# Kernel tuning notes

Measured on AMD Instinct MI355X. Metric: run time of the kernel, lower is better.

Reference implementation:

```python
import jax, jax.numpy as jnp
import numpy as np

EPS = 1e-12
SAMPLE_SIZES = (100, 50)  # hardcoded in the torch module


def setup_inputs() -> dict:
    key = jax.random.key(0)
    k1, k2, k3, k4 = jax.random.split(key, 4)
    N, E, C_IN, C_HID, C_OUT = 50000, 1600000, 256, 64, 128
    x = jax.random.normal(k1, (N, C_IN), dtype=jnp.float32)
    edge_index = jax.random.randint(k2, (2, E), 0, N, dtype=jnp.int64)
    W1 = jax.random.normal(k3, (C_IN, C_HID), dtype=jnp.float32) / np.sqrt(C_IN)
    b1 = jnp.zeros((C_HID,), dtype=jnp.float32)
    W2 = jax.random.normal(k4, (C_HID, C_OUT), dtype=jnp.float32) / np.sqrt(C_HID)
    b2 = jnp.zeros((C_OUT,), dtype=jnp.float32)
    return {"x": x, "edge_index": edge_index, "W1": W1, "b1": b1, "W2": W2, "b2": b2}


def _sample_mask(edge_index, num_samples, key):
    """Keep at most num_samples random out-edges per source node (fixed-shape mask)."""
    src = edge_index[0]
    E = src.shape[0]
    pri = jax.random.uniform(key, (E,))
    order = jnp.lexsort((pri, src))            # group by src, random order within group
    src_sorted = src[order]
    first = jnp.searchsorted(src_sorted, src_sorted, side="left")
    rank = jnp.arange(E) - first               # rank within each src group
    keep_sorted = rank < num_samples
    mask = jnp.zeros((E,), dtype=jnp.float32).at[order].set(keep_sorted.astype(jnp.float32))
    return mask


def _gcn_conv(x, edge_index, edge_weight, W, b, num_nodes):
    """PyG GCNConv: self-loops + symmetric deg^-1/2 normalization, aggregate at dst."""
    h = x @ W                                   # [N, out]
    src, dst = edge_index[0], edge_index[1]
    loop = jnp.arange(num_nodes, dtype=src.dtype)
    src_f = jnp.concatenate([src, loop])
    dst_f = jnp.concatenate([dst, loop])
    w_f = jnp.concatenate([edge_weight, jnp.ones((num_nodes,), dtype=edge_weight.dtype)])
    deg = jax.ops.segment_sum(w_f, dst_f, num_segments=num_nodes)
    dinv = jnp.where(deg > 0, jax.lax.rsqrt(jnp.maximum(deg, EPS)), 0.0)
    norm = w_f * dinv[src_f] * dinv[dst_f]      # [E+N]
    msgs = h[src_f] * norm[:, None]             # gather + scale (memory bound)
    out = jax.ops.segment_sum(msgs, dst_f, num_segments=num_nodes)
    return out + b


def reference(x, edge_index, W1, b1, W2, b2):
    num_nodes = x.shape[0]
    skey = jax.random.key(42)
    sk1, sk2 = jax.random.split(skey)
    m1 = _sample_mask(edge_index, SAMPLE_SIZES[0], sk1)
    m2 = _sample_mask(edge_index, SAMPLE_SIZES[1], sk2)
    h = _gcn_conv(x, edge_index, m1, W1, b1, num_nodes)
    h = jax.nn.relu(h)
    h = h / jnp.maximum(jnp.linalg.norm(h, axis=-1, keepdims=True), EPS)  # F.normalize(p=2)
    out = _gcn_conv(h, edge_index, m2, W2, b2, num_nodes)
    return out
```

## Files before the change

kernel.cpp:

```cpp
#include <hip/hip_runtime.h>

typedef unsigned int u32;
typedef unsigned short u16;
typedef unsigned long long u64;
typedef __attribute__((ext_vector_type(8))) short bh8;
typedef __attribute__((ext_vector_type(4))) float f4;

#define HMAX 1024
#define MAXD 128
#define SB_CAP 24576
#define DB_CAP 6144
#define SBCHUNK 8192
#define SPLIT 8
#define G1S 72
#define DROP_CAP 32768
#define CPAD 16

__device__ inline f4 mfma16(bh8 a, bh8 b, f4 c) {
  return __builtin_amdgcn_mfma_f32_16x16x32_bf16(a, b, c, 0, 0, 0);
}

__host__ __device__ inline void tf2x32(u32 k0, u32 k1, u32 x0, u32 x1, u32& o0, u32& o1) {
  u32 ks2 = k0 ^ k1 ^ 0x1BD11BDAu;
#define ROTL32(x,d) (((x)<<(d))|((x)>>(32-(d))))
#define TFR(r) { x0 += x1; x1 = ROTL32(x1,(r)); x1 ^= x0; }
  x0 += k0; x1 += k1;
  TFR(13) TFR(15) TFR(26) TFR(6)
  x0 += k1; x1 += ks2 + 1u;
  TFR(17) TFR(29) TFR(16) TFR(24)
  x0 += ks2; x1 += k0 + 2u;
  TFR(13) TFR(15) TFR(26) TFR(6)
  x0 += k0; x1 += k1 + 3u;
  TFR(17) TFR(29) TFR(16) TFR(24)
  x0 += k1; x1 += ks2 + 4u;
  TFR(13) TFR(15) TFR(26) TFR(6)
  x0 += ks2; x1 += k0 + 5u;
  o0 = x0; o1 = x1;
#undef TFR
#undef ROTL32
}

__device__ inline u16 f2bf(float f) {
  u32 u = __float_as_uint(f);
  return (u16)((u + 0x7FFFu + ((u >> 16) & 1u)) >> 16);
}
__device__ inline float bflo(u32 u) { return __uint_as_float(u << 16); }
__device__ inline float bfhi(u32 u) { return __uint_as_float(u & 0xFFFF0000u); }

struct BinS { u32 lsrc[128]; u32 lbase[128]; u32 ldst[512]; u32 dbase[512]; };
struct GemS { u16 xs[64 * G1S]; u16 ws[64 * G1S]; };

__global__ __launch_bounds__(256) void k_mega1(const int* __restrict__ ei, int E,
                                               const float* __restrict__ x, int N,
                                               const float* __restrict__ W1, const float* __restrict__ W2,
                                               int* __restrict__ srcCnt, u32* __restrict__ srcRec,
                                               int* __restrict__ dstCnt, u64* __restrict__ dstRec,
                                               u16* __restrict__ h1b, u16* __restrict__ W2t, int nBin) {
  __shared__ __align__(16) char smem[sizeof(GemS)];
  int t = threadIdx.x;
  int bid = blockIdx.x;
  int nGemm = (N + 63) >> 6;

  if (bid < nBin) {
    BinS& S = *(BinS*)smem;
    if (t < 128) S.lsrc[t] = 0;
    for (int v = t; v < 512; v += 256) S.ldst[v] = 0;
    __syncthreads();
    int lo = bid * SBCHUNK;
    int hi = min(lo + SBCHUNK, E);
    bool fast = ((E & 3) == 0);

    auto loadE = [&](int e0, int nv, int* sv, int* dv) {
      if (nv == 8 && fast) {
        int4 a0 = *((const int4*)(ei + e0));
        int4 a1 = *((const int4*)(ei + e0 + 4));
        int4 b0 = *((const int4*)(ei + E + e0));
        int4 b1 = *((const int4*)(ei + E + e0 + 4));
        sv[0]=a0.x; sv[1]=a0.y; sv[2]=a0.z; sv[3]=a0.w; sv[4]=a1.x; sv[5]=a1.y; sv[6]=a1.z; sv[7]=a1.w;
        dv[0]=b0.x; dv[1]=b0.y; dv[2]=b0.z; dv[3]=b0.w; dv[4]=b1.x; dv[5]=b1.y; dv[6]=b1.z; dv[7]=b1.w;
      } else {
        for (int j = 0; j < nv; ++j) { sv[j] = ei[e0 + j]; dv[j] = ei[E + e0 + j]; }
      }
    };

    for (int sub = 0; sub < SBCHUNK; sub += 2048) {
      int e0 = lo + sub + 8 * t;
      int nv = min(8, hi - e0); if (nv < 0) nv = 0;
      int sv[8], dv[8];
      loadE(e0, nv, sv, dv);
      for (int j = 0; j < nv; ++j) {
        atomicAdd(&S.lsrc[sv[j] >> 9], 1u);
        atomicAdd(&S.ldst[dv[j] >> 7], 1u);
      }
    }
    __syncthreads();
    if (t < 128) {
      u32 c = S.lsrc[t];
      if (c) S.lbase[t] = (u32)atomicAdd(&srcCnt[t * CPAD], (int)c);
      S.lsrc[t] = 0;
    }
    for (int v = t; v < 512; v += 256) {
      u32 cd = S.ldst[v];
      if (cd) S.dbase[v] = (u32)atomicAdd(&dstCnt[v * CPAD], (int)cd);
      S.ldst[v] = 0;
    }
    __syncthreads();
    for (int sub = 0; sub < SBCHUNK; sub += 2048) {
      int e0 = lo + sub + 8 * t;
      int nv = min(8, hi - e0); if (nv < 0) nv = 0;
      int sv[8], dv[8];
      loadE(e0, nv, sv, dv);
      for (int j = 0; j < nv; ++j) {
        int s = sv[j], d = dv[j];
        u32 i = (u32)(e0 + j);
        int bs = s >> 9;
        u32 slot = S.lbase[bs] + atomicAdd(&S.lsrc[bs], 1u);
        if (slot < SB_CAP) srcRec[(size_t)bs * SB_CAP + slot] = ((u32)(s & 511) << 21) | i;
        int bd = d >> 7;
        u32 slot2 = S.dbase[bd] + atomicAdd(&S.ldst[bd], 1u);
        if (slot2 < DB_CAP)
          dstRec[(size_t)bd * DB_CAP + slot2] = ((u64)(d & 127) << 37) | ((u64)(u32)s << 21) | i;
      }
    }
  } else if (bid < nBin + nGemm) {
    GemS& G = *(GemS*)smem;
    int wv = t >> 6, lane = t & 63;
    int qd = lane >> 4, md = lane & 15;
    int m0 = (bid - nBin) * 64;
    if (m0 >= N) return;
    f4 acc[4] = {};
    for (int ks = 0; ks < 256; ks += 64) {
      __syncthreads();
#pragma unroll
      for (int i = 0; i < 4; ++i) {
        int f = t + 256 * i;
        int r = f >> 4, c4 = f & 15;
        int grow = m0 + r; if (grow >= N) grow = N - 1;
        float4 v = ((const float4*)x)[(size_t)grow * 64 + (ks >> 2) + c4];
        u32 p0 = (u32)f2bf(v.x) | ((u32)f2bf(v.y) << 16);
        u32 p1 = (u32)f2bf(v.z) | ((u32)f2bf(v.w) << 16);
        *((uint2*)(G.xs + r * G1S + c4 * 4)) = make_uint2(p0, p1);
      }
#pragma unroll
      for (int i = 0; i < 4; ++i) {
        int f = t + 256 * i;
        int k = f >> 4, c4 = f & 15;
        float4 v = ((const float4*)W1)[(ks + k) * 16 + c4];
        int n0 = c4 * 4;
        G.ws[(n0 + 0) * G1S + k] = f2bf(v.x);
        G.ws[(n0 + 1) * G1S + k] = f2bf(v.y);
        G.ws[(n0 + 2) * G1S + k] = f2bf(v.z);
        G.ws[(n0 + 3) * G1S + k] = f2bf(v.w);
      }
      __syncthreads();
#pragma unroll
      for (int kk = 0; kk < 64; kk += 32) {
        bh8 af = *((const bh8*)(G.xs + (16 * wv + md) * G1S + kk + qd * 8));
#pragma unroll
        for (int nt = 0; nt < 4; ++nt) {
          bh8 bf = *((const bh8*)(G.ws + (nt * 16 + md) * G1S + kk + qd * 8));
          acc[nt] = mfma16(af, bf, acc[nt]);
        }
      }
    }
#pragma unroll
    for (int nt = 0; nt < 4; ++nt)
#pragma unroll
      for (int r = 0; r < 4; ++r) {
        int row = m0 + 16 * wv + qd * 4 + r;
        if (row < N) h1b[(size_t)row * 64 + nt * 16 + md] = f2bf(acc[nt][r]);
      }
  } else {
    for (int e = t; e < 64 * 128; e += 256) {
      int n = e & 127, k = e >> 7;
      W2t[n * 64 + k] = f2bf(W2[k * 128 + n]);
    }
  }
}

__global__ __launch_bounds__(256) void k_shist(const int* __restrict__ srcCnt, const u32* __restrict__ srcRec,
                                               int* __restrict__ outdegB) {
  int bk = blockIdx.x >> 3;
  int part = blockIdx.x & (SPLIT - 1);
  int total = min(srcCnt[bk * CPAD], SB_CAP);
  int lo = total * part / SPLIT;
  int hi = total * (part + 1) / SPLIT;
  __shared__ u32 cnt[512];
  int t = threadIdx.x;
  cnt[t] = 0; cnt[t + 256] = 0;
  __syncthreads();
  const u32* R = srcRec + (size_t)bk * SB_CAP;
  for (int i = lo + t; i < hi; i += 256) atomicAdd(&cnt[R[i] >> 21], 1u);
  __syncthreads();
  int base = bk * 512;
  for (int v = t; v < 512; v += 256) {
    u32 c = cnt[v];
    if (c) atomicAdd(&outdegB[base + v], (int)c);
  }
}

__global__ __launch_bounds__(256) void k_hdetect(const int* __restrict__ outdegB, u32* __restrict__ idAB,
                                                 int* __restrict__ hcA, int* __restrict__ hcB,
                                                 const int* __restrict__ dstCnt, int* __restrict__ bucketBase,
                                                 int* __restrict__ dptr, int nbD, int N) {
  int t = threadIdx.x;
  if (blockIdx.x == 0) {
    __shared__ int sc[512], tp[512];
    for (int i = t; i < 512; i += 256) sc[i] = (i < nbD) ? min(dstCnt[i * CPAD], DB_CAP) : 0;
    __syncthreads();
    for (int off = 1; off < 512; off <<= 1) {
      for (int i = t; i < 512; i += 256) tp[i] = sc[i] + ((i >= off) ? sc[i - off] : 0);
      __syncthreads();
      for (int i = t; i < 512; i += 256) sc[i] = tp[i];
      __syncthreads();
    }
    for (int i = t; i < 512; i += 256) {
      if (i < nbD) bucketBase[i] = (i == 0) ? 0 : sc[i - 1];
    }
    if (t == 0) {
      int tot = sc[nbD - 1];
      bucketBase[nbD] = tot;
      dptr[N] = tot;
    }
  }
  int v = blockIdx.x * 256 + t;
  if (v >= N) return;
  int dg = outdegB[v];
  u32 pk = 0;
  if (dg > 50) {
    int idb = atomicAdd(hcB, 1);
    if (idb < HMAX) pk = (u32)(idb + 1);
    if (dg > 100) {
      int ida = atomicAdd(hcA, 1);
      if (ida < HMAX) pk |= (u32)(ida + 1) << 16;
    }
  }
  idAB[v] = pk;
}

__global__ __launch_bounds__(256) void k_hfill(const int* __restrict__ srcCnt, const u32* __restrict__ srcRec,
                                               const u32* __restrict__ idAB,
                                               int* __restrict__ bcA, u64* __restrict__ bukA,
                                               int* __restrict__ bcB, u64* __restrict__ bukB,
                                               u32 kaA, u32 kbA, u32 kaB, u32 kbB) {
  int bk = blockIdx.x >> 3;
  int part = blockIdx.x & (SPLIT - 1);
  int total = min(srcCnt[bk * CPAD], SB_CAP);
  int lo = total * part / SPLIT;
  int hi = total * (part + 1) / SPLIT;
  const u32* R = srcRec + (size_t)bk * SB_CAP;
  int base = bk * 512;
  for (int i = lo + threadIdx.x; i < hi; i += 256) {
    u32 r = R[i];
    u32 pk = idAB[base + (int)(r >> 21)];
    if (pk) {
      u32 e = r & 0x1FFFFFu;
      int idb = (int)(pk & 0xFFFFu) - 1;
      if (idb >= 0) {
        u32 w0, w1; tf2x32(kaB, kbB, 0u, e, w0, w1);
        int slot = atomicAdd(&bcB[idb], 1);
        if (slot < MAXD) bukB[(size_t)idb * MAXD + slot] = ((u64)((w0 ^ w1) >> 9) << 32) | e;
      }
      int ida = (int)(pk >> 16) - 1;
      if (ida >= 0) {
        u32 w0, w1; tf2x32(kaA, kbA, 0u, e, w0, w1);
        int slot = atomicAdd(&bcA[ida], 1);
        if (slot < MAXD) bukA[(size_t)ida * MAXD + slot] = ((u64)((w0 ^ w1) >> 9) << 32) | e;
      }
    }
  }
}

__global__ __launch_bounds__(256) void k_rank2(const int* __restrict__ hcA, const int* __restrict__ bcA,
                                               const u64* __restrict__ bukA,
                                               const int* __restrict__ hcB, const int* __restrict__ bcB,
                                               const u64* __restrict__ bukB,
                                               int* __restrict__ dropCnt, u32* __restrict__ dropList) {
  bool isA = blockIdx.x < (HMAX / 4);
  int bx = isA ? blockIdx.x : blockIdx.x - HMAX / 4;
  const int* hcount = isA ? hcA : hcB;
  const int* bcount = isA ? bcA : bcB;
  const u64* bucket = isA ? bukA : bukB;
  int S = isA ? 100 : 50;
  u32 bit = isA ? 1u : 2u;
  int wid = (bx * 256 + (int)threadIdx.x) >> 6;
  int lane = threadIdx.x & 63;
  int hc = hcount[0]; if (hc > HMAX) hc = HMAX;
  if (wid >= hc) return;
  int d = bcount[wid]; if (d > MAXD) d = MAXD;
  const u64* B = bucket + (size_t)wid * MAXD;
  for (int i = lane; i < d; i += 64) {
    u64 ki = B[i];
    int rank = 0;
    for (int j = 0; j < d; ++j) rank += (B[j] < ki) ? 1 : 0;
    if (rank >= S) {
      int idx = atomicAdd(dropCnt, 1);
      if (idx < DROP_CAP) dropList[idx] = ((u32)ki & 0x1FFFFFu) | (bit << 21);
    }
  }
}

__global__ __launch_bounds__(256) void k_phase2(const int* __restrict__ bucketBase,
                                                const int* __restrict__ dstCnt,
                                                const u64* __restrict__ dstRec,
                                                const int* __restrict__ dropCnt,
                                                const u32* __restrict__ dropList,
                                                u32* __restrict__ entries, int* __restrict__ dptr,
                                                float* __restrict__ dinv1, float* __restrict__ dinv2, int N) {
  int b = blockIdx.x;
  int base = bucketBase[b];
  int cnt0 = min(dstCnt[b * CPAD], DB_CAP);
  const u64* R = dstRec + (size_t)b * DB_CAP;
  __shared__ u32 cnt[128];
  __shared__ u32 htab[4096];
  __shared__ u32 ws2[2];
  int t = threadIdx.x;
  if (t < 128) cnt[t] = 0;
  for (int i = t; i < 4096; i += 256) htab[i] = 0xFFFFFFFFu;
  __syncthreads();
  int dc = min(dropCnt[0], 3072);
  for (int i = t; i < dc; i += 256) {
    u32 pk = dropList[i];
    u32 key = pk & 0x1FFFFFu;
    u32 h = (key * 2654435761u) >> 20;
    while (true) {
      u32 old = atomicCAS(&htab[h], 0xFFFFFFFFu, pk);
      if (old == 0xFFFFFFFFu) break;
      if ((old & 0x1FFFFFu) == key) { atomicOr(&htab[h], pk & 0x00600000u); break; }
      h = (h + 1) & 4095;
    }
  }
  __syncthreads();
  for (int i = t; i < cnt0; i += 256) {
    u64 r = R[i];
    u32 dl = (u32)(r >> 37) & 127u;
    u32 key = (u32)r & 0x1FFFFFu;
    u32 drop = 0;
    u32 h = (key * 2654435761u) >> 20;
    while (true) {
      u32 v = htab[h];
      if (v == 0xFFFFFFFFu) break;
      if ((v & 0x1FFFFFu) == key) { drop = (v >> 21) & 3u; break; }
      h = (h + 1) & 4095;
    }
    u32 add = 1u + ((1u - (drop & 1u)) << 10) + ((1u - ((drop >> 1) & 1u)) << 20);
    atomicAdd(&cnt[dl], add);
  }
  __syncthreads();
  u32 c0 = (t < 128) ? cnt[t] : 0;
  u32 tot = c0 & 1023u;
  int lane = t & 63, w = t >> 6;
  u32 incl = tot;
  for (int off = 1; off < 64; off <<= 1) {
    u32 nbv = (u32)__shfl_up((int)incl, off, 64);
    if (lane >= off) incl += nbv;
  }
  if (lane == 63 && w == 0) ws2[0] = incl;
  __syncthreads();
  u32 excl = incl - tot + ((w == 1) ? ws2[0] : 0u);
  int v0 = b * 128 + t;
  if (t < 128 && v0 < N) {
    dptr[v0] = base + (int)excl;
    dinv1[v0] = 1.0f / sqrtf((float)(((c0 >> 10) & 1023u) + 1u));
    dinv2[v0] = 1.0f / sqrtf((float)(((c0 >> 20) & 1023u) + 1u));
  }
  __syncthreads();
  if (t < 128) cnt[t] = excl;
  __syncthreads();
  for (int i = t; i < cnt0; i += 256) {
    u64 r = R[i];
    u32 dl = (u32)(r >> 37) & 127u;
    u32 key = (u32)r & 0x1FFFFFu;
    u32 drop = 0;
    u32 h = (key * 2654435761u) >> 20;
    while (true) {
      u32 v = htab[h];
      if (v == 0xFFFFFFFFu) break;
      if ((v & 0x1FFFFFu) == key) { drop = (v >> 21) & 3u; break; }
      h = (h + 1) & 4095;
    }
    u32 src = (u32)(r >> 21) & 0xFFFFu;
    u32 slot = atomicAdd(&cnt[dl], 1u);
    entries[base + slot] = src | ((drop & 1u) ? 0u : (1u << 30)) | ((drop & 2u) ? 0u : (1u << 31));
  }
}

__global__ __launch_bounds__(256) void k_conv1n(const int* __restrict__ ptr, const u32* __restrict__ entries,
                                                const float* __restrict__ dinv1, const uint4* __restrict__ h1q,
                                                const float* __restrict__ b1, uint4* __restrict__ hnbq, int N) {
  int wid = (blockIdx.x * 256 + threadIdx.x) >> 6;
  if (wid >= N) return;
  int lane = threadIdx.x & 63;
  int lo8 = lane & 7, grp = lane >> 3;
  int beg = ptr[wid], end = ptr[wid + 1];
  float a0 = 0.f, a1 = 0.f, a2 = 0.f, a3 = 0.f, a4 = 0.f, a5 = 0.f, a6 = 0.f, a7 = 0.f;
  for (int cb = beg; cb < end; cb += 64) {
    int idx = cb + lane;
    float wgt = 0.f; int s = 0;
    if (idx < end) {
      u32 e = entries[idx];
      s = (int)(e & 0xFFFFu);
      if (e & (1u << 30)) wgt = dinv1[s];
    }
    int nq = (min(64, end - cb) + 7) >> 3;
    int j = grp;
    float w = __shfl(wgt, j, 64);
    int sj = __shfl(s, j, 64);
    uint4 uv = h1q[(size_t)sj * 8 + lo8];
    for (int i = 1; i < nq; ++i) {
      int j2 = j + 8;
      float w2 = __shfl(wgt, j2, 64);
      int s2 = __shfl(s, j2, 64);
      uint4 uv2 = h1q[(size_t)s2 * 8 + lo8];
      a0 = fmaf(w, bflo(uv.x), a0); a1 = fmaf(w, bfhi(uv.x), a1);
      a2 = fmaf(w, bflo(uv.y), a2); a3 = fmaf(w, bfhi(uv.y), a3);
      a4 = fmaf(w, bflo(uv.z), a4); a5 = fmaf(w, bfhi(uv.z), a5);
      a6 = fmaf(w, bflo(uv.w), a6); a7 = fmaf(w, bfhi(uv.w), a7);
      w = w2; uv = uv2; j = j2;
    }
    a0 = fmaf(w, bflo(uv.x), a0); a1 = fmaf(w, bfhi(uv.x), a1);
    a2 = fmaf(w, bflo(uv.y), a2); a3 = fmaf(w, bfhi(uv.y), a3);
    a4 = fmaf(w, bflo(uv.z), a4); a5 = fmaf(w, bfhi(uv.z), a5);
    a6 = fmaf(w, bflo(uv.w), a6); a7 = fmaf(w, bfhi(uv.w), a7);
  }
#pragma unroll
  for (int off = 8; off < 64; off <<= 1) {
    a0 += __shfl_xor(a0, off, 64); a1 += __shfl_xor(a1, off, 64);
    a2 += __shfl_xor(a2, off, 64); a3 += __shfl_xor(a3, off, 64);
    a4 += __shfl_xor(a4, off, 64); a5 += __shfl_xor(a5, off, 64);
    a6 += __shfl_xor(a6, off, 64); a7 += __shfl_xor(a7, off, 64);
  }
  float dv = dinv1[wid];
  uint4 uo = h1q[(size_t)wid * 8 + lo8];
  a0 = fmaf(dv, bflo(uo.x), a0); a1 = fmaf(dv, bfhi(uo.x), a1);
  a2 = fmaf(dv, bflo(uo.y), a2); a3 = fmaf(dv, bfhi(uo.y), a3);
  a4 = fmaf(dv, bflo(uo.z), a4); a5 = fmaf(dv, bfhi(uo.z), a5);
  a6 = fmaf(dv, bflo(uo.w), a6); a7 = fmaf(dv, bfhi(uo.w), a7);
  float4 bbA = ((const float4*)b1)[lo8 * 2];
  float4 bbB = ((const float4*)b1)[lo8 * 2 + 1];
  float o0 = fmaxf(fmaf(dv, a0, bbA.x), 0.f);
  float o1 = fmaxf(fmaf(dv, a1, bbA.y), 0.f);
  float o2 = fmaxf(fmaf(dv, a2, bbA.z), 0.f);
  float o3 = fmaxf(fmaf(dv, a3, bbA.w), 0.f);
  float o4 = fmaxf(fmaf(dv, a4, bbB.x), 0.f);
  float o5 = fmaxf(fmaf(dv, a5, bbB.y), 0.f);
  float o6 = fmaxf(fmaf(dv, a6, bbB.z), 0.f);
  float o7 = fmaxf(fmaf(dv, a7, bbB.w), 0.f);
  float ss = fmaf(o0, o0, fmaf(o1, o1, fmaf(o2, o2, o3 * o3)))
           + fmaf(o4, o4, fmaf(o5, o5, fmaf(o6, o6, o7 * o7)));
#pragma unroll
  for (int off = 1; off < 8; off <<= 1) ss += __shfl_xor(ss, off, 8);
  float sc = 1.f / fmaxf(sqrtf(ss), 1e-12f);
  if (lane < 8) {
    uint4 pv;
    pv.x = (u32)f2bf(o0 * sc) | ((u32)f2bf(o1 * sc) << 16);
    pv.y = (u32)f2bf(o2 * sc) | ((u32)f2bf(o3 * sc) << 16);
    pv.z = (u32)f2bf(o4 * sc) | ((u32)f2bf(o5 * sc) << 16);
    pv.w = (u32)f2bf(o6 * sc) | ((u32)f2bf(o7 * sc) << 16);
    hnbq[(size_t)wid * 8 + lo8] = pv;
  }
}

__global__ __launch_bounds__(256) void k_agg2(const int* __restrict__ ptr, const u32* __restrict__ entries,
                                              const float* __restrict__ dinv2, const uint4* __restrict__ hnq,
                                              uint4* __restrict__ agg2q, int N) {
  int wid = (blockIdx.x * 256 + threadIdx.x) >> 6;
  if (wid >= N) return;
  int lane = threadIdx.x & 63;
  int lo8 = lane & 7, grp = lane >> 3;
  int beg = ptr[wid], end = ptr[wid + 1];
  float a0 = 0.f, a1 = 0.f, a2 = 0.f, a3 = 0.f, a4 = 0.f, a5 = 0.f, a6 = 0.f, a7 = 0.f;
  for (int cb = beg; cb < end; cb += 64) {
    int idx = cb + lane;
    float wgt = 0.f; int s = 0;
    if (idx < end) {
      u32 e = entries[idx];
      s = (int)(e & 0xFFFFu);
      if (e & (1u << 31)) wgt = dinv2[s];
    }
    int nq = (min(64, end - cb) + 7) >> 3;
    int j = grp;
    float w = __shfl(wgt, j, 64);
    int sj = __shfl(s, j, 64);
    uint4 uv = hnq[(size_t)sj * 8 + lo8];
    for (int i = 1; i < nq; ++i) {
      int j2 = j + 8;
      float w2 = __shfl(wgt, j2, 64);
      int s2 = __shfl(s, j2, 64);
      uint4 uv2 = hnq[(size_t)s2 * 8 + lo8];
      a0 = fmaf(w, bflo(uv.x), a0); a1 = fmaf(w, bfhi(uv.x), a1);
      a2 = fmaf(w, bflo(uv.y), a2); a3 = fmaf(w, bfhi(uv.y), a3);
      a4 = fmaf(w, bflo(uv.z), a4); a5 = fmaf(w, bfhi(uv.z), a5);
      a6 = fmaf(w, bflo(uv.w), a6); a7 = fmaf(w, bfhi(uv.w), a7);
      w = w2; uv = uv2; j = j2;
    }
    a0 = fmaf(w, bflo(uv.x), a0); a1 = fmaf(w, bfhi(uv.x), a1);
    a2 = fmaf(w, bflo(uv.y), a2); a3 = fmaf(w, bfhi(uv.y), a3);
    a4 = fmaf(w, bflo(uv.z), a4); a5 = fmaf(w, bfhi(uv.z), a5);
    a6 = fmaf(w, bflo(uv.w), a6); a7 = fmaf(w, bfhi(uv.w), a7);
  }
#pragma unroll
  for (int off = 8; off < 64; off <<= 1) {
    a0 += __shfl_xor(a0, off, 64); a1 += __shfl_xor(a1, off, 64);
    a2 += __shfl_xor(a2, off, 64); a3 += __shfl_xor(a3, off, 64);
    a4 += __shfl_xor(a4, off, 64); a5 += __shfl_xor(a5, off, 64);
    a6 += __shfl_xor(a6, off, 64); a7 += __shfl_xor(a7, off, 64);
  }
  float dv = dinv2[wid];
  uint4 uo = hnq[(size_t)wid * 8 + lo8];
  a0 = fmaf(dv, bflo(uo.x), a0); a1 = fmaf(dv, bfhi(uo.x), a1);
  a2 = fmaf(dv, bflo(uo.y), a2); a3 = fmaf(dv, bfhi(uo.y), a3);
  a4 = fmaf(dv, bflo(uo.z), a4); a5 = fmaf(dv, bfhi(uo.z), a5);
  a6 = fmaf(dv, bflo(uo.w), a6); a7 = fmaf(dv, bfhi(uo.w), a7);
  if (lane < 8) {
    uint4 pv;
    pv.x = (u32)f2bf(dv * a0) | ((u32)f2bf(dv * a1) << 16);
    pv.y = (u32)f2bf(dv * a2) | ((u32)f2bf(dv * a3) << 16);
    pv.z = (u32)f2bf(dv * a4) | ((u32)f2bf(dv * a5) << 16);
    pv.w = (u32)f2bf(dv * a6) | ((u32)f2bf(dv * a7) << 16);
    agg2q[(size_t)wid * 8 + lo8] = pv;
  }
}

#define G2S 72
__global__ __launch_bounds__(256) void k_gemm2f(const u16* __restrict__ aggb, const u16* __restrict__ W2t,
                                                const float* __restrict__ b2, float* __restrict__ out, int N) {
  __shared__ u16 hs[64 * G2S];
  __shared__ u16 ws[128 * G2S];
  int t = threadIdx.x;
  int wv = t >> 6, lane = t & 63;
  int qd = lane >> 4, md = lane & 15;
  int m0 = blockIdx.x * 64;
#pragma unroll
  for (int i = 0; i < 2; ++i) {
    int cc = t + 256 * i;
    int r = cc >> 3, kc = (cc & 7) * 8;
    int grow = m0 + r; if (grow >= N) grow = N - 1;
    *((uint4*)(hs + r * G2S + kc)) = *((const uint4*)(aggb + (size_t)grow * 64 + kc));
  }
#pragma unroll
  for (int i = 0; i < 4; ++i) {
    int cc = t + 256 * i;
    int n = cc >> 3, kc = (cc & 7) * 8;
    *((uint4*)(ws + n * G2S + kc)) = *((const uint4*)(W2t + n * 64 + kc));
  }
  __syncthreads();
  f4 acc[8] = {};
#pragma unroll
  for (int kk = 0; kk < 64; kk += 32) {
    bh8 af = *((const bh8*)(hs + (16 * wv + md) * G2S + kk + qd * 8));
#pragma unroll
    for (int nt = 0; nt < 8; ++nt) {
      bh8 bf = *((const bh8*)(ws + (nt * 16 + md) * G2S + kk + qd * 8));
      acc[nt] = mfma16(af, bf, acc[nt]);
    }
  }
#pragma unroll
  for (int nt = 0; nt < 8; ++nt) {
    float bv = b2[nt * 16 + md];
#pragma unroll
    for (int r = 0; r < 4; ++r) {
      int row = m0 + 16 * wv + qd * 4 + r;
      if (row < N) out[(size_t)row * 128 + nt * 16 + md] = acc[nt][r] + bv;
    }
  }
}

extern "C" void kernel_launch(void* const* d_in, const int* in_sizes, int n_in,
                              void* d_out, int out_size, void* d_ws, size_t ws_size,
                              hipStream_t stream) {
  const float* x  = (const float*)d_in[0];
  const int*   ei = (const int*)d_in[1];
  const float* W1 = (const float*)d_in[2];
  const float* b1 = (const float*)d_in[3];
  const float* W2 = (const float*)d_in[4];
  const float* b2 = (const float*)d_in[5];
  const int N = in_sizes[0] / 256;
  const int E = in_sizes[1] / 2;
  const int nbS = (N + 511) >> 9;
  const int nbD = (N + 127) >> 7;

  u32 sk1a, sk1b, sk2a, sk2b;
  tf2x32(0u, 42u, 0u, 0u, sk1a, sk1b);
  tf2x32(0u, 42u, 0u, 1u, sk2a, sk2b);

  char* p = (char*)d_ws;
  auto alloc = [&](size_t bytes) { char* r = p; p += (bytes + 255) & ~(size_t)255; return r; };
  int* dstCnt      = (int*)alloc((size_t)512 * CPAD * 4);
  int* srcCnt      = (int*)alloc((size_t)128 * CPAD * 4);
  int* hcbA        = (int*)alloc((size_t)(1 + HMAX) * 4);
  int* hcbB        = (int*)alloc((size_t)(1 + HMAX) * 4);
  int* outdegB     = (int*)alloc((size_t)nbS * 512 * 4);
  int* dropCnt     = (int*)alloc(256);
  char* zero_end = p;
  u32* dropList = (u32*)alloc((size_t)DROP_CAP * 4);
  u32* idAB     = (u32*)alloc((size_t)nbS * 512 * 4);
  u16* h1b      = (u16*)alloc((size_t)N * 64 * 2);
  u16* hnb      = (u16*)alloc((size_t)N * 64 * 2);
  u16* agg2b    = (u16*)alloc((size_t)N * 64 * 2);
  float* dinv1  = (float*)alloc((size_t)N * 4);
  float* dinv2  = (float*)alloc((size_t)N * 4);
  int* dptr     = (int*)alloc((size_t)(N + 1) * 4);
  int* bucketBase = (int*)alloc(513 * 4);
  u32* entries  = (u32*)alloc((size_t)E * 4);
  u32* srcRec   = (u32*)alloc((size_t)nbS * SB_CAP * 4);
  u64* dstRec   = (u64*)alloc((size_t)nbD * DB_CAP * 8);
  u64* bukA     = (u64*)alloc((size_t)HMAX * MAXD * 8);
  u64* bukB     = (u64*)alloc((size_t)HMAX * MAXD * 8);
  u16* W2t      = (u16*)alloc(64 * 128 * 2);

  int* hcA = hcbA; int* bcA = hcbA + 1;
  int* hcB = hcbB; int* bcB = hcbB + 1;

  hipMemsetAsync(dstCnt, 0x00, (size_t)(zero_end - (char*)dstCnt), stream);

  const int nBin = (E + SBCHUNK - 1) / SBCHUNK;
  const int nGemm = (N + 63) / 64;
  k_mega1<<<nBin + nGemm + 1, 256, 0, stream>>>(ei, E, x, N, W1, W2,
                                                srcCnt, srcRec, dstCnt, dstRec, h1b, W2t, nBin);
  k_shist<<<nbS * SPLIT, 256, 0, stream>>>(srcCnt, srcRec, outdegB);
  k_hdetect<<<(N + 255) / 256, 256, 0, stream>>>(outdegB, idAB, hcA, hcB, dstCnt, bucketBase,
                                                 dptr, nbD, N);
  k_hfill<<<nbS * SPLIT, 256, 0, stream>>>(srcCnt, srcRec, idAB, bcA, bukA, bcB, bukB,
                                           sk1a, sk1b, sk2a, sk2b);
  k_rank2<<<HMAX / 2, 256, 0, stream>>>(hcA, bcA, bukA, hcB, bcB, bukB, dropCnt, dropList);
  k_phase2<<<nbD, 256, 0, stream>>>(bucketBase, dstCnt, dstRec, dropCnt, dropList,
                                    entries, dptr, dinv1, dinv2, N);
  k_conv1n<<<(N * 64 + 255) / 256, 256, 0, stream>>>(dptr, entries, dinv1, (const uint4*)h1b, b1,
                                                     (uint4*)hnb, N);
  k_agg2<<<(N * 64 + 255) / 256, 256, 0, stream>>>(dptr, entries, dinv2, (const uint4*)hnb,
                                                   (uint4*)agg2b, N);
  k_gemm2f<<<(N + 63) / 64, 256, 0, stream>>>(agg2b, W2t, b2, (float*)d_out, N);
}
```

Baseline: 264.1 us.

## Cache edges in registers, memoize drop lookups in LDS, deepen gather prefetch

The binning pass now loads each thread's 32 edges into registers once and reuses them for both the counting and scatter passes, instead of reading edge_index from global memory twice. In phase2, each record's source, drop flags and local destination are packed into a shared-memory array on the first pass, so the second pass neither rereads the global records nor repeats the hash-table probe. Both aggregation kernels now keep two feature gathers in flight instead of one, to hide gather latency. The trade-offs are extra register pressure in the binning path and about 24KB of extra LDS in phase2, which may reduce occupancy.

```diff
diff --git a/kernel.cpp b/kernel.cpp
--- a/kernel.cpp
+++ b/kernel.cpp
@@ -47,6 +47,12 @@
 __device__ inline float bflo(u32 u) { return __uint_as_float(u << 16); }
 __device__ inline float bfhi(u32 u) { return __uint_as_float(u & 0xFFFF0000u); }
 
+#define ACC8(uv, wt) \
+  a0 = fmaf(wt, bflo(uv.x), a0); a1 = fmaf(wt, bfhi(uv.x), a1); \
+  a2 = fmaf(wt, bflo(uv.y), a2); a3 = fmaf(wt, bfhi(uv.y), a3); \
+  a4 = fmaf(wt, bflo(uv.z), a4); a5 = fmaf(wt, bfhi(uv.z), a5); \
+  a6 = fmaf(wt, bflo(uv.w), a6); a7 = fmaf(wt, bfhi(uv.w), a7);
+
 struct BinS { u32 lsrc[128]; u32 lbase[128]; u32 ldst[512]; u32 dbase[512]; };
 struct GemS { u16 xs[64 * G1S]; u16 ws[64 * G1S]; };
 
@@ -69,28 +75,32 @@
     int lo = bid * SBCHUNK;
     int hi = min(lo + SBCHUNK, E);
     bool fast = ((E & 3) == 0);
-
-    auto loadE = [&](int e0, int nv, int* sv, int* dv) {
+    int sv[32], dv[32];
+#pragma unroll
+    for (int sub = 0; sub < 4; ++sub) {
+      int e0 = lo + sub * 2048 + 8 * t;
+      int nv = min(8, hi - e0); if (nv < 0) nv = 0;
       if (nv == 8 && fast) {
         int4 a0 = *((const int4*)(ei + e0));
         int4 a1 = *((const int4*)(ei + e0 + 4));
         int4 b0 = *((const int4*)(ei + E + e0));
         int4 b1 = *((const int4*)(ei + E + e0 + 4));
-        sv[0]=a0.x; sv[1]=a0.y; sv[2]=a0.z; sv[3]=a0.w; sv[4]=a1.x; sv[5]=a1.y; sv[6]=a1.z; sv[7]=a1.w;
-        dv[0]=b0.x; dv[1]=b0.y; dv[2]=b0.z; dv[3]=b0.w; dv[4]=b1.x; dv[5]=b1.y; dv[6]=b1.z; dv[7]=b1.w;
+        sv[sub*8+0]=a0.x; sv[sub*8+1]=a0.y; sv[sub*8+2]=a0.z; sv[sub*8+3]=a0.w;
+        sv[sub*8+4]=a1.x; sv[sub*8+5]=a1.y; sv[sub*8+6]=a1.z; sv[sub*8+7]=a1.w;
+        dv[sub*8+0]=b0.x; dv[sub*8+1]=b0.y; dv[sub*8+2]=b0.z; dv[sub*8+3]=b0.w;
+        dv[sub*8+4]=b1.x; dv[sub*8+5]=b1.y; dv[sub*8+6]=b1.z; dv[sub*8+7]=b1.w;
       } else {
-        for (int j = 0; j < nv; ++j) { sv[j] = ei[e0 + j]; dv[j] = ei[E + e0 + j]; }
-      }
-    };
-
-    for (int sub = 0; sub < SBCHUNK; sub += 2048) {
-      int e0 = lo + sub + 8 * t;
-      int nv = min(8, hi - e0); if (nv < 0) nv = 0;
-      int sv[8], dv[8];
-      loadE(e0, nv, sv, dv);
-      for (int j = 0; j < nv; ++j) {
-        atomicAdd(&S.lsrc[sv[j] >> 9], 1u);
-        atomicAdd(&S.ldst[dv[j] >> 7], 1u);
+#pragma unroll
+        for (int j = 0; j < 8; ++j) {
+          int s_ = 0, d_ = 0;
+          if (j < nv) { s_ = ei[e0 + j]; d_ = ei[E + e0 + j]; }
+          sv[sub*8+j] = s_; dv[sub*8+j] = d_;
+        }
+      }
+#pragma unroll
+      for (int j = 0; j < 8; ++j) if (j < nv) {
+        atomicAdd(&S.lsrc[sv[sub*8+j] >> 9], 1u);
+        atomicAdd(&S.ldst[dv[sub*8+j] >> 7], 1u);
       }
     }
     __syncthreads();
@@ -105,13 +115,13 @@
       S.ldst[v] = 0;
     }
     __syncthreads();
-    for (int sub = 0; sub < SBCHUNK; sub += 2048) {
-      int e0 = lo + sub + 8 * t;
+#pragma unroll
+    for (int sub = 0; sub < 4; ++sub) {
+      int e0 = lo + sub * 2048 + 8 * t;
       int nv = min(8, hi - e0); if (nv < 0) nv = 0;
-      int sv[8], dv[8];
-      loadE(e0, nv, sv, dv);
-      for (int j = 0; j < nv; ++j) {
-        int s = sv[j], d = dv[j];
+#pragma unroll
+      for (int j = 0; j < 8; ++j) if (j < nv) {
+        int s = sv[sub*8+j], d = dv[sub*8+j];
         u32 i = (u32)(e0 + j);
         int bs = s >> 9;
         u32 slot = S.lbase[bs] + atomicAdd(&S.lsrc[bs], 1u);
@@ -314,6 +324,7 @@
   __shared__ u32 cnt[128];
   __shared__ u32 htab[4096];
   __shared__ u32 ws2[2];
+  __shared__ u32 earr[DB_CAP];
   int t = threadIdx.x;
   if (t < 128) cnt[t] = 0;
   for (int i = t; i < 4096; i += 256) htab[i] = 0xFFFFFFFFu;
@@ -343,6 +354,8 @@
       if ((v & 0x1FFFFFu) == key) { drop = (v >> 21) & 3u; break; }
       h = (h + 1) & 4095;
     }
+    u32 src = (u32)(r >> 21) & 0xFFFFu;
+    earr[i] = src | (drop << 16) | (dl << 18);
     u32 add = 1u + ((1u - (drop & 1u)) << 10) + ((1u - ((drop >> 1) & 1u)) << 20);
     atomicAdd(&cnt[dl], add);
   }
@@ -368,18 +381,10 @@
   if (t < 128) cnt[t] = excl;
   __syncthreads();
   for (int i = t; i < cnt0; i += 256) {
-    u64 r = R[i];
-    u32 dl = (u32)(r >> 37) & 127u;
-    u32 key = (u32)r & 0x1FFFFFu;
-    u32 drop = 0;
-    u32 h = (key * 2654435761u) >> 20;
-    while (true) {
-      u32 v = htab[h];
-      if (v == 0xFFFFFFFFu) break;
-      if ((v & 0x1FFFFFu) == key) { drop = (v >> 21) & 3u; break; }
-      h = (h + 1) & 4095;
-    }
-    u32 src = (u32)(r >> 21) & 0xFFFFu;
+    u32 p = earr[i];
+    u32 dl = (p >> 18) & 127u;
+    u32 drop = (p >> 16) & 3u;
+    u32 src = p & 0xFFFFu;
     u32 slot = atomicAdd(&cnt[dl], 1u);
     entries[base + slot] = src | ((drop & 1u) ? 0u : (1u << 30)) | ((drop & 2u) ? 0u : (1u << 31));
   }
@@ -403,25 +408,22 @@
       if (e & (1u << 30)) wgt = dinv1[s];
     }
     int nq = (min(64, end - cb) + 7) >> 3;
-    int j = grp;
-    float w = __shfl(wgt, j, 64);
-    int sj = __shfl(s, j, 64);
-    uint4 uv = h1q[(size_t)sj * 8 + lo8];
-    for (int i = 1; i < nq; ++i) {
-      int j2 = j + 8;
-      float w2 = __shfl(wgt, j2, 64);
-      int s2 = __shfl(s, j2, 64);
-      uint4 uv2 = h1q[(size_t)s2 * 8 + lo8];
-      a0 = fmaf(w, bflo(uv.x), a0); a1 = fmaf(w, bfhi(uv.x), a1);
-      a2 = fmaf(w, bflo(uv.y), a2); a3 = fmaf(w, bfhi(uv.y), a3);
-      a4 = fmaf(w, bflo(uv.z), a4); a5 = fmaf(w, bfhi(uv.z), a5);
-      a6 = fmaf(w, bflo(uv.w), a6); a7 = fmaf(w, bfhi(uv.w), a7);
-      w = w2; uv = uv2; j = j2;
-    }
-    a0 = fmaf(w, bflo(uv.x), a0); a1 = fmaf(w, bfhi(uv.x), a1);
-    a2 = fmaf(w, bflo(uv.y), a2); a3 = fmaf(w, bfhi(uv.y), a3);
-    a4 = fmaf(w, bflo(uv.z), a4); a5 = fmaf(w, bfhi(uv.z), a5);
-    a6 = fmaf(w, bflo(uv.w), a6); a7 = fmaf(w, bfhi(uv.w), a7);
+    float wA = __shfl(wgt, grp, 64); int sA = __shfl(s, grp, 64);
+    uint4 uA = h1q[(size_t)sA * 8 + lo8];
+    float wB = 0.f; uint4 uB = uA;
+    if (nq > 1) {
+      wB = __shfl(wgt, grp + 8, 64); int sB = __shfl(s, grp + 8, 64);
+      uB = h1q[(size_t)sB * 8 + lo8];
+    }
+    for (int i = 2; i < nq; ++i) {
+      int jc = grp + 8 * i;
+      float wC = __shfl(wgt, jc, 64); int sC = __shfl(s, jc, 64);
+      uint4 uC = h1q[(size_t)sC * 8 + lo8];
+      ACC8(uA, wA)
+      wA = wB; uA = uB; wB = wC; uB = uC;
+    }
+    ACC8(uA, wA)
+    if (nq > 1) { ACC8(uB, wB) }
   }
 #pragma unroll
   for (int off = 8; off < 64; off <<= 1) {
@@ -479,25 +481,22 @@
       if (e & (1u << 31)) wgt = dinv2[s];
     }
     int nq = (min(64, end - cb) + 7) >> 3;
-    int j = grp;
-    float w = __shfl(wgt, j, 64);
-    int sj = __shfl(s, j, 64);
-    uint4 uv = hnq[(size_t)sj * 8 + lo8];
-    for (int i = 1; i < nq; ++i) {
-      int j2 = j + 8;
-      float w2 = __shfl(wgt, j2, 64);
-      int s2 = __shfl(s, j2, 64);
-      uint4 uv2 = hnq[(size_t)s2 * 8 + lo8];
-      a0 = fmaf(w, bflo(uv.x), a0); a1 = fmaf(w, bfhi(uv.x), a1);
-      a2 = fmaf(w, bflo(uv.y), a2); a3 = fmaf(w, bfhi(uv.y), a3);
-      a4 = fmaf(w, bflo(uv.z), a4); a5 = fmaf(w, bfhi(uv.z), a5);
-      a6 = fmaf(w, bflo(uv.w), a6); a7 = fmaf(w, bfhi(uv.w), a7);
-      w = w2; uv = uv2; j = j2;
-    }
-    a0 = fmaf(w, bflo(uv.x), a0); a1 = fmaf(w, bfhi(uv.x), a1);
-    a2 = fmaf(w, bflo(uv.y), a2); a3 = fmaf(w, bfhi(uv.y), a3);
-    a4 = fmaf(w, bflo(uv.z), a4); a5 = fmaf(w, bfhi(uv.z), a5);
-    a6 = fmaf(w, bflo(uv.w), a6); a7 = fmaf(w, bfhi(uv.w), a7);
+    float wA = __shfl(wgt, grp, 64); int sA = __shfl(s, grp, 64);
+    uint4 uA = hnq[(size_t)sA * 8 + lo8];
+    float wB = 0.f; uint4 uB = uA;
+    if (nq > 1) {
+      wB = __shfl(wgt, grp + 8, 64); int sB = __shfl(s, grp + 8, 64);
+      uB = hnq[(size_t)sB * 8 + lo8];
+    }
+    for (int i = 2; i < nq; ++i) {
+      int jc = grp + 8 * i;
+      float wC = __shfl(wgt, jc, 64); int sC = __shfl(s, jc, 64);
+      uint4 uC = hnq[(size_t)sC * 8 + lo8];
+      ACC8(uA, wA)
+      wA = wB; uA = uB; wB = wC; uB = uC;
+    }
+    ACC8(uA, wA)
+    if (nq > 1) { ACC8(uB, wB) }
   }
 #pragma unroll
   for (int off = 8; off < 64; off <<= 1) {
```

Measured after the change: 266.1 us. Within noise of the previous version (+0.8%).
